# Kernel tuning notes

Hardware: AMD Instinct MI355X
Metric: run time of the kernel (lower is better)

## Reference

```python
import jax, jax.numpy as jnp
import numpy as np


def conv1x1(x, w, b):
    # x: [b,c,h,w], w: [o,c], b: [o]
    return jnp.einsum('bchw,oc->bohw', x, w) + b[None, :, None, None]


def maxpool2(x):
    b, c, h, w = x.shape
    return x.reshape(b, c, h // 2, 2, w // 2, 2).max(axis=(3, 5))


def setup_inputs() -> dict:
    key = jax.random.key(0)
    ks = jax.random.split(key, 10)
    c = 64
    x = jax.random.normal(ks[0], (16, c, 64, 64), dtype=jnp.float32)
    s = 0.05
    wf = jax.random.normal(ks[1], (c // 8, c), dtype=jnp.float32) * s
    bf = jax.random.normal(ks[2], (c // 8,), dtype=jnp.float32) * s
    wg = jax.random.normal(ks[3], (c // 8, c), dtype=jnp.float32) * s
    bg = jax.random.normal(ks[4], (c // 8,), dtype=jnp.float32) * s
    wh = jax.random.normal(ks[5], (c // 2, c), dtype=jnp.float32) * s
    bh = jax.random.normal(ks[6], (c // 2,), dtype=jnp.float32) * s
    wv = jax.random.normal(ks[7], (c, c // 2), dtype=jnp.float32) * s
    bv = jax.random.normal(ks[8], (c,), dtype=jnp.float32) * s
    gamma = jax.random.normal(ks[9], (1,), dtype=jnp.float32)
    return {'x': x, 'wf': wf, 'bf': bf, 'wg': wg, 'bg': bg,
            'wh': wh, 'bh': bh, 'wv': wv, 'bv': bv, 'gamma': gamma}


def reference(x, wf, bf, wg, bg, wh, bh, wv, bv, gamma):
    b, c, h, w = x.shape
    n = h * w          # query length
    m = n // 4         # key/value length after 2x2 maxpool
    # query branch: f(x) -> [b, c//8, n]
    fx = conv1x1(x, wf, bf).reshape(b, c // 8, n)
    # key branch: maxpool(g(x)) -> [b, c//8, m]
    gx = maxpool2(conv1x1(x, wg, bg)).reshape(b, c // 8, m)
    # attention: [b, n, m]
    attn = jax.nn.softmax(jnp.einsum('bcn,bcm->bnm', fx, gx), axis=-1)
    # value branch: maxpool(h(x)) -> [b, c//2, m]
    hx = maxpool2(conv1x1(x, wh, bh)).reshape(b, c // 2, m)
    # merge: [b, c//2, n] -> [b, c//2, h, w]
    merged = jnp.einsum('bnm,bcm->bcn', attn, hx).reshape(b, c // 2, h, w)
    return x + gamma[0] * conv1x1(merged, wv, bv)
```

## Files before the change

kernel.cpp:

```cpp
#include <hip/hip_runtime.h>
#include <hip/hip_bf16.h>
#include <math.h>

#define BB 16
#define CC 64
#define HW 4096
#define MM 1024
#define CK 8
#define CV 32
#define LOG2E 1.4426950408889634f

typedef float f32x4 __attribute__((ext_vector_type(4)));
typedef short s16x8 __attribute__((ext_vector_type(8)));

union U4 { uint4 u; s16x8 s; };

__device__ inline unsigned short bfu(float a) {
    __hip_bfloat16 h = __float2bfloat16(a);
    union { __hip_bfloat16 h; unsigned short u; } c; c.h = h; return c.u;
}
__device__ inline unsigned int pk2bf(float a, float b) {
    return (unsigned int)bfu(a) | ((unsigned int)bfu(b) << 16);
}
__device__ inline unsigned int pk2bf_t(float a, float b) {
    return (__float_as_uint(a) >> 16) | (__float_as_uint(b) & 0xffff0000u);
}

#define FXB_OFF 0
#define GXA_OFF 1048576
#define HXC_OFF 1310720
#define WVB_OFF 2359296

__global__ __launch_bounds__(256, 6) void prep_kernel(
    const float* __restrict__ x,
    const float* __restrict__ wf, const float* __restrict__ bf,
    const float* __restrict__ wg, const float* __restrict__ bg,
    const float* __restrict__ wh, const float* __restrict__ bh,
    const float* __restrict__ wv,
    unsigned short* __restrict__ fxB, unsigned short* __restrict__ gxA,
    unsigned short* __restrict__ hxC, unsigned short* __restrict__ wvB)
{
    __shared__ __align__(16) float wsm[8 * CC];
    __shared__ __align__(16) unsigned short sHp[64][8];

    int tid   = threadIdx.x;
    int chunk = blockIdx.y;
    const float* wsrc = (chunk == 0) ? wf : (chunk == 1) ? wg : (wh + (size_t)(chunk - 2) * 8 * CC);
    const float* bsrc = (chunk == 0) ? bf : (chunk == 1) ? bg : (bh + (chunk - 2) * 8);

    for (int i = tid; i < 8 * CC; i += 256) wsm[i] = wsrc[i];

    if (blockIdx.x == 0 && chunk == 0) {
        int t = tid >> 6, ll = tid & 63;
        const float* wr = wv + (size_t)(t * 16 + (ll & 15)) * CV + ((ll >> 4) * 8);
        uint4 wu;
        wu.x = pk2bf(wr[0], wr[1]); wu.y = pk2bf(wr[2], wr[3]);
        wu.z = pk2bf(wr[4], wr[5]); wu.w = pk2bf(wr[6], wr[7]);
        *(uint4*)(wvB + (size_t)tid * 8) = wu;
    }
    __syncthreads();

    int wave = tid >> 6, l = tid & 63;
    int wp = blockIdx.x * 4 + wave;
    int b  = wp >> 6;
    int t2 = wp & 63;
    int rpair = t2 >> 1, chalf = t2 & 1;
    int col = chalf * 32 + (l >> 2) * 2 + (l & 1);
    int row = rpair * 2 + ((l >> 1) & 1);
    int pix = row * 64 + col;

    float o8[8];
#pragma unroll
    for (int o = 0; o < 8; ++o) o8[o] = bsrc[o];

    const float* xp = x + (size_t)b * CC * HW + pix;
#pragma unroll 4
    for (int c4 = 0; c4 < CC; c4 += 4) {
        float v0 = xp[(c4 + 0) * HW];
        float v1 = xp[(c4 + 1) * HW];
        float v2 = xp[(c4 + 2) * HW];
        float v3 = xp[(c4 + 3) * HW];
#pragma unroll
        for (int o = 0; o < 8; ++o) {
            float4 w = *(const float4*)&wsm[o * CC + c4];
            o8[o] = fmaf(w.x, v0, fmaf(w.y, v1, fmaf(w.z, v2, fmaf(w.w, v3, o8[o]))));
        }
    }

    if (chunk == 0) {
        uint4 fu;
        fu.x = pk2bf(o8[0] * LOG2E, o8[1] * LOG2E);
        fu.y = pk2bf(o8[2] * LOG2E, o8[3] * LOG2E);
        fu.z = pk2bf(o8[4] * LOG2E, o8[5] * LOG2E);
        fu.w = pk2bf(o8[6] * LOG2E, o8[7] * LOG2E);
        *(uint4*)(fxB + (size_t)(b * HW + pix) * CK) = fu;
    } else {
#pragma unroll
        for (int o = 0; o < 8; ++o) {
            o8[o] = fmaxf(o8[o], __shfl_xor(o8[o], 1, 64));
            o8[o] = fmaxf(o8[o], __shfl_xor(o8[o], 2, 64));
        }
        int ppl = l >> 2;
        if (chunk == 1) {
            if ((l & 3) == 0) {
                uint4 gu;
                gu.x = pk2bf(o8[0], o8[1]); gu.y = pk2bf(o8[2], o8[3]);
                gu.z = pk2bf(o8[4], o8[5]); gu.w = pk2bf(o8[6], o8[7]);
                *(uint4*)(gxA + (size_t)(b * MM + t2 * 16 + ppl) * CK) = gu;
            }
        } else {
            if ((l & 3) == 0) {
                uint4 hu;
                hu.x = pk2bf(o8[0], o8[1]); hu.y = pk2bf(o8[2], o8[3]);
                hu.z = pk2bf(o8[4], o8[5]); hu.w = pk2bf(o8[6], o8[7]);
                *(uint4*)&sHp[wave * 16 + ppl][0] = hu;
            }
            __syncthreads();
            int ch = tid >> 5, j = tid & 31;
            unsigned int v = (unsigned int)sHp[2 * j][ch]
                           | ((unsigned int)sHp[2 * j + 1][ch] << 16);
            int ppb = (blockIdx.x * 4 & 63) * 16;
            int chg = (chunk - 2) * 8 + ch;
            *(unsigned int*)(hxC + (size_t)(b * CV + chg) * MM + ppb + 2 * j) = v;
        }
    }
}

__global__ __launch_bounds__(512, 4) void attn_kernel(
    const float* __restrict__ x,
    const unsigned short* __restrict__ fxB, const unsigned short* __restrict__ gxA,
    const unsigned short* __restrict__ hxC, const unsigned short* __restrict__ wvB,
    const float* __restrict__ bv, const float* __restrict__ gamma,
    float* __restrict__ out)
{
    __shared__ float sAcc[4][4][8][64];
    __shared__ float sSum[4][4][64];

    int tid = threadIdx.x;
    int l   = tid & 63;
    int w   = tid >> 6;
    int qg  = w >> 2;
    int kq  = w & 3;
    int b   = blockIdx.x >> 6;
    int qb  = (blockIdx.x & 63) * 64;
    int q16 = l & 15;
    int h   = l >> 4;
    int prm = ((q16 & 12) << 1) | (q16 & 3);
    bool lo16 = (l < 16);

    U4 qf[2];
#pragma unroll
    for (int j = 0; j < 2; ++j) {
        int qt = qg * 2 + j;
        uint4 v = *(const uint4*)(fxB + (size_t)(b * HW + qb + qt * 16 + q16) * CK);
        if (!lo16) { v.x = 0; v.y = 0; v.z = 0; v.w = 0; }
        qf[j].u = v;
    }

    f32x4 zz = {0.f, 0.f, 0.f, 0.f};
    f32x4 acc0[2] = {zz, zz}, acc1[2] = {zz, zz};
    float ssum[2] = {0.f, 0.f};

    const unsigned short* gxb = gxA + (size_t)b * MM * CK;
    const unsigned short* hxb = hxC + (size_t)b * CV * MM;

#pragma unroll 2
    for (int gi = 0; gi < 8; ++gi) {
        int g = kq * 8 + gi;
        U4 ga, gb2, v0, v1;
        ga.u  = *(const uint4*)(gxb + (size_t)(g * 32 + prm) * CK);
        gb2.u = *(const uint4*)(gxb + (size_t)(g * 32 + prm + 4) * CK);
        v0.u  = *(const uint4*)(hxb + (size_t)(prm)     * MM + g * 32 + h * 8);
        v1.u  = *(const uint4*)(hxb + (size_t)(prm + 4) * MM + g * 32 + h * 8);

#pragma unroll
        for (int j = 0; j < 2; ++j) {
            f32x4 s0 = __builtin_amdgcn_mfma_f32_16x16x32_bf16(ga.s,  qf[j].s, zz, 0, 0, 0);
            f32x4 s1 = __builtin_amdgcn_mfma_f32_16x16x32_bf16(gb2.s, qf[j].s, zz, 0, 0, 0);
            float e0 = __builtin_exp2f(s0.x), e1 = __builtin_exp2f(s0.y);
            float e2 = __builtin_exp2f(s0.z), e3 = __builtin_exp2f(s0.w);
            float e4 = __builtin_exp2f(s1.x), e5 = __builtin_exp2f(s1.y);
            float e6 = __builtin_exp2f(s1.z), e7 = __builtin_exp2f(s1.w);
            ssum[j] += ((e0 + e1) + (e2 + e3)) + ((e4 + e5) + (e6 + e7));
            U4 bp;
            bp.u.x = pk2bf_t(e0, e1); bp.u.y = pk2bf_t(e2, e3);
            bp.u.z = pk2bf_t(e4, e5); bp.u.w = pk2bf_t(e6, e7);
            acc0[j] = __builtin_amdgcn_mfma_f32_16x16x32_bf16(v0.s, bp.s, acc0[j], 0, 0, 0);
            acc1[j] = __builtin_amdgcn_mfma_f32_16x16x32_bf16(v1.s, bp.s, acc1[j], 0, 0, 0);
        }
    }

#pragma unroll
    for (int j = 0; j < 2; ++j) {
        int qt = qg * 2 + j;
#pragma unroll
        for (int e = 0; e < 4; ++e) {
            sAcc[qt][kq][e][l]     = acc0[j][e];
            sAcc[qt][kq][4 + e][l] = acc1[j][e];
        }
        sSum[qt][kq][l] = ssum[j];
    }
    __syncthreads();

    int qt_f = w & 3;
    int oth  = w >> 2;
    f32x4 ca0 = zz, ca1 = zz;
    float cs = 0.f;
#pragma unroll
    for (int k2 = 0; k2 < 4; ++k2) {
#pragma unroll
        for (int e = 0; e < 4; ++e) {
            ca0[e] += sAcc[qt_f][k2][e][l];
            ca1[e] += sAcc[qt_f][k2][4 + e][l];
        }
        cs += sSum[qt_f][k2][l];
    }
    cs += __shfl_xor(cs, 16, 64);
    cs += __shfl_xor(cs, 32, 64);
    float inv = 1.0f / cs;

    U4 mb;
    mb.u.x = pk2bf_t(ca0.x * inv, ca0.y * inv);
    mb.u.y = pk2bf_t(ca0.z * inv, ca0.w * inv);
    mb.u.z = pk2bf_t(ca1.x * inv, ca1.y * inv);
    mb.u.w = pk2bf_t(ca1.z * inv, ca1.w * inv);

    float gm = gamma[0];
    int q = qb + qt_f * 16 + q16;
    const float* xq = x + (size_t)b * CC * HW + q;
    float*       oq = out + (size_t)b * CC * HW + q;
#pragma unroll
    for (int i = 0; i < 2; ++i) {
        int ot = oth * 2 + i;
        U4 wva;
        wva.u = *(const uint4*)(wvB + (size_t)(ot * 64 + l) * CK);
        f32x4 d = __builtin_amdgcn_mfma_f32_16x16x32_bf16(wva.s, mb.s, zz, 0, 0, 0);
#pragma unroll
        for (int r = 0; r < 4; ++r) {
            int o = ot * 16 + h * 4 + r;
            oq[(size_t)o * HW] = xq[(size_t)o * HW] + gm * (d[r] + bv[o]);
        }
    }
}

extern "C" void kernel_launch(void* const* d_in, const int* in_sizes, int n_in,
                              void* d_out, int out_size, void* d_ws, size_t ws_size,
                              hipStream_t stream) {
    const float* x     = (const float*)d_in[0];
    const float* wf    = (const float*)d_in[1];
    const float* bf    = (const float*)d_in[2];
    const float* wg    = (const float*)d_in[3];
    const float* bg    = (const float*)d_in[4];
    const float* wh    = (const float*)d_in[5];
    const float* bh    = (const float*)d_in[6];
    const float* wv    = (const float*)d_in[7];
    const float* bv    = (const float*)d_in[8];
    const float* gamma = (const float*)d_in[9];
    float* out = (float*)d_out;
    char* ws = (char*)d_ws;

    unsigned short* fxB = (unsigned short*)(ws + FXB_OFF);
    unsigned short* gxA = (unsigned short*)(ws + GXA_OFF);
    unsigned short* hxC = (unsigned short*)(ws + HXC_OFF);
    unsigned short* wvB = (unsigned short*)(ws + WVB_OFF);

    prep_kernel<<<dim3(256, 6), 256, 0, stream>>>(x, wf, bf, wg, bg, wh, bh, wv,
                                                  fxB, gxA, hxC, wvB);
    attn_kernel<<<1024, 512, 0, stream>>>(x, fxB, gxA, hxC, wvB, bv, gamma, out);
}
```

Before: 47.85 us.

## Pre-tile key/value MFMA fragments into contiguous layout via extra kernel

Adds a tile_kernel that gathers the key (gxA) and value (hxC) operands into a per-lane fragment-ordered buffer, so that in the attention inner loop each lane does a fully coalesced contiguous 16-byte load instead of strided, permuted gathers. It removes scattered global loads from the hot loop. The cost is an extra kernel launch and an extra round trip of about 1.3 MB through memory.

```diff
diff --git a/kernel.cpp b/kernel.cpp
--- a/kernel.cpp
+++ b/kernel.cpp
@@ -30,6 +30,7 @@
 #define GXA_OFF 1048576
 #define HXC_OFF 1310720
 #define WVB_OFF 2359296
+#define FRG_OFF 2363392
 
 __global__ __launch_bounds__(256, 6) void prep_kernel(
     const float* __restrict__ x,
@@ -126,10 +127,31 @@
     }
 }
 
+__global__ __launch_bounds__(256) void tile_kernel(
+    const unsigned short* __restrict__ gxA, const unsigned short* __restrict__ hxC,
+    unsigned short* __restrict__ frag)
+{
+    int bg = blockIdx.x;
+    int b  = bg >> 5, g = bg & 31;
+    int tid = threadIdx.x;
+    int which = tid >> 6, l = tid & 63;
+    int q16 = l & 15, h = l >> 4;
+    int prm = ((q16 & 12) << 1) | (q16 & 3);
+
+    const unsigned short* src;
+    if (which < 2) {
+        src = gxA + (size_t)(b * MM + g * 32 + prm + (which ? 4 : 0)) * CK;
+    } else {
+        src = hxC + (size_t)(b * CV + prm + ((which == 3) ? 4 : 0)) * MM + g * 32 + h * 8;
+    }
+    uint4 v = *(const uint4*)src;
+    *(uint4*)(frag + ((size_t)bg * 4 + which) * 64 * 8 + (size_t)l * 8) = v;
+}
+
 __global__ __launch_bounds__(512, 4) void attn_kernel(
     const float* __restrict__ x,
-    const unsigned short* __restrict__ fxB, const unsigned short* __restrict__ gxA,
-    const unsigned short* __restrict__ hxC, const unsigned short* __restrict__ wvB,
+    const unsigned short* __restrict__ fxB, const unsigned short* __restrict__ frag,
+    const unsigned short* __restrict__ wvB,
     const float* __restrict__ bv, const float* __restrict__ gamma,
     float* __restrict__ out)
 {
@@ -145,7 +167,6 @@
     int qb  = (blockIdx.x & 63) * 64;
     int q16 = l & 15;
     int h   = l >> 4;
-    int prm = ((q16 & 12) << 1) | (q16 & 3);
     bool lo16 = (l < 16);
 
     U4 qf[2];
@@ -161,17 +182,16 @@
     f32x4 acc0[2] = {zz, zz}, acc1[2] = {zz, zz};
     float ssum[2] = {0.f, 0.f};
 
-    const unsigned short* gxb = gxA + (size_t)b * MM * CK;
-    const unsigned short* hxb = hxC + (size_t)b * CV * MM;
+    const unsigned short* fb = frag + ((size_t)(b * 32 + kq * 8) * 4) * 64 * 8
+                                    + (size_t)l * 8;
 
 #pragma unroll 2
     for (int gi = 0; gi < 8; ++gi) {
-        int g = kq * 8 + gi;
         U4 ga, gb2, v0, v1;
-        ga.u  = *(const uint4*)(gxb + (size_t)(g * 32 + prm) * CK);
-        gb2.u = *(const uint4*)(gxb + (size_t)(g * 32 + prm + 4) * CK);
-        v0.u  = *(const uint4*)(hxb + (size_t)(prm)     * MM + g * 32 + h * 8);
-        v1.u  = *(const uint4*)(hxb + (size_t)(prm + 4) * MM + g * 32 + h * 8);
+        ga.u  = *(const uint4*)(fb + (size_t)(gi * 4 + 0) * 512);
+        gb2.u = *(const uint4*)(fb + (size_t)(gi * 4 + 1) * 512);
+        v0.u  = *(const uint4*)(fb + (size_t)(gi * 4 + 2) * 512);
+        v1.u  = *(const uint4*)(fb + (size_t)(gi * 4 + 3) * 512);
 
 #pragma unroll
         for (int j = 0; j < 2; ++j) {
@@ -259,12 +279,14 @@
     float* out = (float*)d_out;
     char* ws = (char*)d_ws;
 
-    unsigned short* fxB = (unsigned short*)(ws + FXB_OFF);
-    unsigned short* gxA = (unsigned short*)(ws + GXA_OFF);
-    unsigned short* hxC = (unsigned short*)(ws + HXC_OFF);
-    unsigned short* wvB = (unsigned short*)(ws + WVB_OFF);
+    unsigned short* fxB  = (unsigned short*)(ws + FXB_OFF);
+    unsigned short* gxA  = (unsigned short*)(ws + GXA_OFF);
+    unsigned short* hxC  = (unsigned short*)(ws + HXC_OFF);
+    unsigned short* wvB  = (unsigned short*)(ws + WVB_OFF);
+    unsigned short* frag = (unsigned short*)(ws + FRG_OFF);
 
     prep_kernel<<<dim3(256, 6), 256, 0, stream>>>(x, wf, bf, wg, bg, wh, bh, wv,
                                                   fxB, gxA, hxC, wvB);
-    attn_kernel<<<1024, 512, 0, stream>>>(x, fxB, gxA, hxC, wvB, bv, gamma, out);
-}
+    tile_kernel<<<512, 256, 0, stream>>>(gxA, hxC, frag);
+    attn_kernel<<<1024, 512, 0, stream>>>(x, fxB, frag, wvB, bv, gamma, out);
+}
```

Measured after the change: 48.50 us. No clear change (+1.4%).
